# Performance work log

Hardware: AMD Instinct MI355X
Metric: run time of the kernel (lower is better)

## Reference

```python
import jax, jax.numpy as jnp
import numpy as np

EMBED_DIM = 256
NUM_HEADS = 4
HEAD_DIM = EMBED_DIM // NUM_HEADS
SCALE = HEAD_DIM ** (-0.5)


def setup_inputs() -> dict:
    key = jax.random.key(0)
    kx, kq, kp, kb = jax.random.split(key, 4)
    B, N, C = 4, 4096, EMBED_DIM
    x = jax.random.normal(kx, (B, N, C), dtype=jnp.float32)
    # qkv: Linear(C, 3C, bias=False); torch stores weight as [out, in]
    w_qkv = jax.random.normal(kq, (3 * C, C), dtype=jnp.float32) * (C ** -0.5)
    w_proj = jax.random.normal(kp, (C, C), dtype=jnp.float32) * (C ** -0.5)
    b_proj = jax.random.normal(kb, (C,), dtype=jnp.float32) * 0.01
    return {"x": x, "w_qkv": w_qkv, "w_proj": w_proj, "b_proj": b_proj}


def reference(x, w_qkv, w_proj, b_proj):
    B, N, C = x.shape
    H, D = NUM_HEADS, HEAD_DIM
    # qkv projection: [B,N,3C] -> [3,B,H,N,D]
    qkv = (x @ w_qkv.T).reshape(B, N, 3, H, D).transpose(2, 0, 3, 1, 4)
    q, k, v = qkv[0], qkv[1], qkv[2]
    # materialized [B,H,N,N] scores (faithful to the original)
    attn = jnp.einsum("bhnd,bhmd->bhnm", q, k) * SCALE
    attn_probs = jax.nn.softmax(attn, axis=-1)
    out = jnp.einsum("bhnm,bhmd->bhnd", attn_probs, v)
    out = out.transpose(0, 2, 1, 3).reshape(B, N, C)
    return out @ w_proj.T + b_proj
```

## Files before the change

kernel.cpp:

```cpp
#include <hip/hip_runtime.h>
#include <hip/hip_bf16.h>

typedef __hip_bfloat16 bf16;
typedef _Float16 f16;
typedef __attribute__((ext_vector_type(8))) short bf16x8;
typedef __attribute__((ext_vector_type(8))) _Float16 f16x8;
typedef __attribute__((ext_vector_type(2))) _Float16 f16x2;
typedef __attribute__((ext_vector_type(4))) float f32x4;
typedef __attribute__((ext_vector_type(4))) unsigned int u32x4;
typedef __attribute__((ext_vector_type(2))) unsigned int u32x2;

#define B_ 4
#define N_ 4096
#define C_ 256
#define H_ 4
#define D_ 64
#define KLN 0.18033688011112042f

#if __has_builtin(__builtin_amdgcn_exp2f)
#define EXP2(x) __builtin_amdgcn_exp2f(x)
#else
#define EXP2(x) exp2f(x)
#endif
#if __has_builtin(__builtin_amdgcn_rcpf)
#define RCP(x) __builtin_amdgcn_rcpf(x)
#else
#define RCP(x) (1.0f / (x))
#endif

__device__ inline void load_lds16(const void* g, void* l) {
#if __has_builtin(__builtin_amdgcn_global_load_lds)
    __builtin_amdgcn_global_load_lds(
        (const __attribute__((address_space(1))) unsigned int*)g,
        (__attribute__((address_space(3))) unsigned int*)l, 16, 0, 0);
#else
    int ln = __lane_id();
    ((u32x4*)l)[ln] = *((const u32x4*)g);
#endif
}

__device__ inline unsigned int pk2(float a, float b) {
    unsigned int ua = __builtin_bit_cast(unsigned int, a) + 0x8000u;
    unsigned int ub = __builtin_bit_cast(unsigned int, b) + 0x8000u;
    return (ua >> 16) | (ub & 0xffff0000u);
}
__device__ inline unsigned int pkh2(float a, float b) {
#if __has_builtin(__builtin_amdgcn_cvt_pkrtz)
    return __builtin_bit_cast(unsigned int, __builtin_amdgcn_cvt_pkrtz(a, b));
#else
    f16x2 h = { (f16)a, (f16)b };
    return __builtin_bit_cast(unsigned int, h);
#endif
}
__device__ inline short f2s(float x) {
    return (short)__builtin_bit_cast(unsigned short, __float2bfloat16(x));
}
__device__ inline bf16x8 cvt8(const float* __restrict__ p) {
    f32x4 a = *reinterpret_cast<const f32x4*>(p);
    f32x4 b = *reinterpret_cast<const f32x4*>(p + 4);
    bf16x8 r = { f2s(a[0]), f2s(a[1]), f2s(a[2]), f2s(a[3]),
                 f2s(b[0]), f2s(b[1]), f2s(b[2]), f2s(b[3]) };
    return r;
}

__global__ __launch_bounds__(256) void cast_bf16(const float* __restrict__ x,
                                                 const float* __restrict__ wq,
                                                 const float* __restrict__ wp,
                                                 bf16* __restrict__ xb,
                                                 bf16* __restrict__ wqb,
                                                 bf16* __restrict__ wpb)
{
    int bid = blockIdx.x;
    const float* s; bf16* d; int base;
    if (bid < 2048)      { s = x;  d = xb;  base = bid * 2048; }
    else if (bid < 2144) { s = wq; d = wqb; base = (bid - 2048) * 2048; }
    else                 { s = wp; d = wpb; base = (bid - 2144) * 2048; }
    int i = base + threadIdx.x * 8;
    f32x4 a = *reinterpret_cast<const f32x4*>(s + i);
    f32x4 b = *reinterpret_cast<const f32x4*>(s + i + 4);
    u32x4 o;
    o.x = pk2(a[0], a[1]); o.y = pk2(a[2], a[3]);
    o.z = pk2(b[0], b[1]); o.w = pk2(b[2], b[3]);
    *reinterpret_cast<u32x4*>(d + i) = o;
}

__global__ __launch_bounds__(256, 2) void qkv_fast(const bf16* __restrict__ x,
                                                   const bf16* __restrict__ w,
                                                   bf16* __restrict__ qw,
                                                   bf16* __restrict__ kw,
                                                   f16* __restrict__ vtw)
{
    __shared__ short w_s[64][264];
    const int tid  = threadIdx.x;
    const int lane = tid & 63;
    const int wav  = tid >> 6;
    const int quad = lane >> 4;
    const int l16  = lane & 15;
    const int bid = (blockIdx.x & 7) * 192 + (blockIdx.x >> 3);
    const int mt = bid / 12, nb = bid % 12;
    const int m0 = mt * 128, n0 = nb * 64;

    {
        const int row = tid >> 2, cb = (tid & 3) * 64;
        const bf16* src = w + (size_t)(n0 + row) * C_ + cb;
#pragma unroll
        for (int i = 0; i < 8; ++i)
            *reinterpret_cast<bf16x8*>(&w_s[row][cb + i * 8]) =
                *reinterpret_cast<const bf16x8*>(src + i * 8);
    }
    __syncthreads();

#pragma unroll
    for (int half = 0; half < 2; ++half) {
        const int mh = m0 + half * 64;
        f32x4 acc[4] = {{0,0,0,0},{0,0,0,0},{0,0,0,0},{0,0,0,0}};
        const bf16* xrow = x + (size_t)(mh + wav * 16 + l16) * C_ + quad * 8;
        if (nb < 8) {
#pragma unroll
            for (int k0 = 0; k0 < C_; k0 += 32) {
                bf16x8 a = *reinterpret_cast<const bf16x8*>(xrow + k0);
#pragma unroll
                for (int nt = 0; nt < 4; ++nt) {
                    bf16x8 b = *reinterpret_cast<const bf16x8*>(&w_s[nt * 16 + l16][k0 + quad * 8]);
                    acc[nt] = __builtin_amdgcn_mfma_f32_16x16x32_bf16(b, a, acc[nt], 0, 0, 0);
                }
            }
        } else {
#pragma unroll
            for (int k0 = 0; k0 < C_; k0 += 32) {
                bf16x8 a = *reinterpret_cast<const bf16x8*>(xrow + k0);
#pragma unroll
                for (int nt = 0; nt < 4; ++nt) {
                    bf16x8 b = *reinterpret_cast<const bf16x8*>(&w_s[nt * 16 + l16][k0 + quad * 8]);
                    acc[nt] = __builtin_amdgcn_mfma_f32_16x16x32_bf16(a, b, acc[nt], 0, 0, 0);
                }
            }
        }

        const int bb = mh >> 12;
        const int nbase = (mh + wav * 16) & (N_ - 1);
        if (nb < 4) {
            bf16* dst = qw + (((size_t)bb * H_ + nb) * N_ + nbase + l16) * D_;
#pragma unroll
            for (int nt = 0; nt < 4; ++nt) {
                u32x2 wv = { pk2(acc[nt][0] * KLN, acc[nt][1] * KLN),
                             pk2(acc[nt][2] * KLN, acc[nt][3] * KLN) };
                *reinterpret_cast<u32x2*>(dst + nt * 16 + quad * 4) = wv;
            }
        } else if (nb < 8) {
            bf16* dst = kw + (((size_t)bb * H_ + (nb - 4)) * N_ + nbase + l16) * D_;
#pragma unroll
            for (int nt = 0; nt < 4; ++nt) {
                u32x2 wv = { pk2(acc[nt][0], acc[nt][1]),
                             pk2(acc[nt][2], acc[nt][3]) };
                *reinterpret_cast<u32x2*>(dst + nt * 16 + quad * 4) = wv;
            }
        } else {
            const int h = nb - 8;
#pragma unroll
            for (int nt = 0; nt < 4; ++nt) {
                int d = nt * 16 + l16;
                u32x2 wv;
                wv.x = pkh2(acc[nt][0], acc[nt][1]);
                wv.y = pkh2(acc[nt][2], acc[nt][3]);
                *reinterpret_cast<u32x2*>(
                    vtw + (((size_t)bb * H_ + h) * D_ + d) * N_ + nbase + quad * 4) = wv;
            }
        }
    }
}

__global__ __launch_bounds__(256) void qkv_cvt(const float* __restrict__ x,
                                               const float* __restrict__ w,
                                               bf16* __restrict__ qw,
                                               bf16* __restrict__ kw,
                                               f16* __restrict__ vtw)
{
    const int lane = threadIdx.x & 63;
    const int wav  = threadIdx.x >> 6;
    const int quad = lane >> 4;
    const int l16  = lane & 15;
    const int gw   = blockIdx.x * 4 + wav;
    const int m0   = (gw / 12) * 16;
    const int n0   = (gw % 12) * 64;

    f32x4 acc[4] = {{0,0,0,0},{0,0,0,0},{0,0,0,0},{0,0,0,0}};
    const float* xrow = x + (size_t)(m0 + l16) * C_ + quad * 8;
#pragma unroll
    for (int k0 = 0; k0 < C_; k0 += 32) {
        bf16x8 a = cvt8(xrow + k0);
#pragma unroll
        for (int nt = 0; nt < 4; ++nt) {
            bf16x8 b = cvt8(w + (size_t)(n0 + nt * 16 + l16) * C_ + k0 + quad * 8);
            acc[nt] = __builtin_amdgcn_mfma_f32_16x16x32_bf16(a, b, acc[nt], 0, 0, 0);
        }
    }
#pragma unroll
    for (int nt = 0; nt < 4; ++nt)
#pragma unroll
        for (int r = 0; r < 4; ++r) {
            int m  = m0 + quad * 4 + r;
            int o  = n0 + nt * 16 + l16;
            int bb = m >> 12;
            int n  = m & (N_ - 1);
            if (o < 256) {
                int h = o >> 6, d = o & 63;
                qw[(((size_t)bb * H_ + h) * N_ + n) * D_ + d] =
                    __float2bfloat16(acc[nt][r] * KLN);
            } else if (o < 512) {
                int oo = o - 256; int h = oo >> 6, d = oo & 63;
                kw[(((size_t)bb * H_ + h) * N_ + n) * D_ + d] =
                    __float2bfloat16(acc[nt][r]);
            } else {
                int oo = o - 512; int h = oo >> 6, d = oo & 63;
                vtw[(((size_t)bb * H_ + h) * D_ + d) * N_ + n] = (f16)acc[nt][r];
            }
        }
}

__global__ __launch_bounds__(512, 4) void attn(const bf16* __restrict__ q,
                                               const bf16* __restrict__ k,
                                               const f16* __restrict__ vt,
                                               bf16* __restrict__ o)
{
    __shared__ __align__(16) char smem[65536];
    short* k_s = reinterpret_cast<short*>(smem);
    f16*   v_s = reinterpret_cast<f16*>(smem + 32768);

    const int tid  = threadIdx.x;
    const int lane = tid & 63;
    const int wav  = tid >> 6;
    const int quad = lane >> 4;
    const int l16  = lane & 15;
    const int l8   = lane & 7;
    const int sub  = wav & 3;
    const int jh   = wav >> 2;

    const int wg = (blockIdx.x & 7) * 64 + (blockIdx.x >> 3);
    const int bh = wg >> 5;
    const int qt = wg & 31;
    const int bb = bh >> 2, h = bh & 3;

    const bf16* qp = q  + (size_t)bh * N_ * D_;
    const bf16* kp = k  + (size_t)bh * N_ * D_;
    const f16*  vp = vt + (size_t)bh * D_ * N_;

    const int qbase = qt * 128 + sub * 32;
    bf16x8 qb[2][2];
#pragma unroll
    for (int qg = 0; qg < 2; ++qg)
#pragma unroll
        for (int ks = 0; ks < 2; ++ks)
            qb[qg][ks] = *reinterpret_cast<const bf16x8*>(
                qp + (size_t)(qbase + qg * 16 + l16) * D_ + ks * 32 + quad * 8);

    const int ri = lane >> 3;
    const int ci = lane & 7;
    const int gc = ci ^ ri;
    int koff[2], voff[2], lds_r[2];
#pragma unroll
    for (int g = 0; g < 2; ++g) {
        const int rb  = sub * 16 + g * 8;
        const int rho = rb + ri;
        const int pr  = (rho & 32) | ((rho & 12) << 1) | ((rho & 16) >> 2) | (rho & 3);
        koff[g]  = pr * D_ + gc * 8;
        voff[g]  = rho * N_ + gc * 8;
        lds_r[g] = rb * 64;
    }

    f32x4 oacc[2][4];
    f32x4 lv[2];
#pragma unroll
    for (int qg = 0; qg < 2; ++qg) {
        lv[qg] = (f32x4){0, 0, 0, 0};
#pragma unroll
        for (int dt = 0; dt < 4; ++dt) oacc[qg][dt] = (f32x4){0, 0, 0, 0};
    }

    auto stage = [&](int buf, int t) {
        const int j0 = jh * 2048 + t * 64;
        short* kd = k_s + (size_t)(buf * 2 + jh) * 4096;
        f16*   vd = v_s + (size_t)(buf * 2 + jh) * 4096;
#pragma unroll
        for (int g = 0; g < 2; ++g) {
            load_lds16(kp + (size_t)j0 * D_ + koff[g], kd + lds_r[g]);
            load_lds16(vp + j0 + voff[g],              vd + lds_r[g]);
        }
    };

    stage(0, 0);
    __syncthreads();

    for (int t = 0; t < 32; ++t) {
        const int cur = t & 1;
        if (t < 31) stage(cur ^ 1, t + 1);

        const short* kt  = k_s + (size_t)(cur * 2 + jh) * 4096;
        const f16*   vtl = v_s + (size_t)(cur * 2 + jh) * 4096;

        f32x4 s[2][4];
        __builtin_amdgcn_s_setprio(1);
#pragma unroll
        for (int nt = 0; nt < 4; ++nt) {
            const int rb = (nt * 16 + l16) * 64;
            bf16x8 k0 = *reinterpret_cast<const bf16x8*>(kt + rb + ((quad    ) ^ l8) * 8);
            bf16x8 k1 = *reinterpret_cast<const bf16x8*>(kt + rb + ((4 + quad) ^ l8) * 8);
#pragma unroll
            for (int qg = 0; qg < 2; ++qg) {
                s[qg][nt] = __builtin_amdgcn_mfma_f32_16x16x32_bf16(
                    k0, qb[qg][0], (f32x4){0.f, 0.f, 0.f, 0.f}, 0, 0, 0);
                s[qg][nt] = __builtin_amdgcn_mfma_f32_16x16x32_bf16(
                    k1, qb[qg][1], s[qg][nt], 0, 0, 0);
            }
        }
        __builtin_amdgcn_s_setprio(0);

        f16x8 pb[2][2];
#pragma unroll
        for (int qg = 0; qg < 2; ++qg)
#pragma unroll
            for (int ks = 0; ks < 2; ++ks) {
                const f32x4 sa = s[qg][2 * ks], sb = s[qg][2 * ks + 1];
                f32x4 pa = { EXP2(sa[0]), EXP2(sa[1]), EXP2(sa[2]), EXP2(sa[3]) };
                f32x4 pc = { EXP2(sb[0]), EXP2(sb[1]), EXP2(sb[2]), EXP2(sb[3]) };
                u32x4 pw;
                pw.x = pkh2(pa[0], pa[1]);
                pw.y = pkh2(pa[2], pa[3]);
                pw.z = pkh2(pc[0], pc[1]);
                pw.w = pkh2(pc[2], pc[3]);
                pb[qg][ks] = __builtin_bit_cast(f16x8, pw);
                lv[qg] += pa;
                lv[qg] += pc;
            }

        __builtin_amdgcn_s_setprio(1);
#pragma unroll
        for (int ks = 0; ks < 2; ++ks)
#pragma unroll
            for (int dt = 0; dt < 4; ++dt) {
                f16x8 va = *reinterpret_cast<const f16x8*>(
                    vtl + (dt * 16 + l16) * 64 + (((ks << 2) + quad) ^ l8) * 8);
#pragma unroll
                for (int qg = 0; qg < 2; ++qg)
                    oacc[qg][dt] = __builtin_amdgcn_mfma_f32_16x16x32_f16(va, pb[qg][ks], oacc[qg][dt], 0, 0, 0);
            }
        __builtin_amdgcn_s_setprio(0);

        __syncthreads();
    }

    float lr[2];
#pragma unroll
    for (int qg = 0; qg < 2; ++qg) {
        float l = (lv[qg][0] + lv[qg][1]) + (lv[qg][2] + lv[qg][3]);
        l += __shfl_xor(l, 16);
        l += __shfl_xor(l, 32);
        lr[qg] = l;
    }

    float* mrg = reinterpret_cast<float*>(smem);
    const int slot = (sub * 64 + lane) * 35;
    if (jh == 1) {
#pragma unroll
        for (int qg = 0; qg < 2; ++qg) {
#pragma unroll
            for (int dt = 0; dt < 4; ++dt)
#pragma unroll
                for (int e = 0; e < 4; ++e)
                    mrg[slot + qg * 17 + dt * 4 + e] = oacc[qg][dt][e];
            mrg[slot + qg * 17 + 16] = lr[qg];
        }
    }
    __syncthreads();
    if (jh == 0) {
#pragma unroll
        for (int qg = 0; qg < 2; ++qg) {
            const float rl = RCP(lr[qg] + mrg[slot + qg * 17 + 16]);
            const size_t obase = ((size_t)bb * N_ + qbase + qg * 16 + l16) * C_ + h * D_;
#pragma unroll
            for (int dt = 0; dt < 4; ++dt) {
                float v0 = (oacc[qg][dt][0] + mrg[slot + qg * 17 + dt * 4 + 0]) * rl;
                float v1 = (oacc[qg][dt][1] + mrg[slot + qg * 17 + dt * 4 + 1]) * rl;
                float v2 = (oacc[qg][dt][2] + mrg[slot + qg * 17 + dt * 4 + 2]) * rl;
                float v3 = (oacc[qg][dt][3] + mrg[slot + qg * 17 + dt * 4 + 3]) * rl;
                u32x2 wv = { pk2(v0, v1), pk2(v2, v3) };
                *reinterpret_cast<u32x2*>(o + obase + dt * 16 + quad * 4) = wv;
            }
        }
    }
}

__global__ __launch_bounds__(256, 2) void out_proj_fast(const bf16* __restrict__ ov,
                                                        const bf16* __restrict__ w,
                                                        const float* __restrict__ bias,
                                                        float* __restrict__ out)
{
    __shared__ short w_s[64][264];
    const int tid  = threadIdx.x;
    const int lane = tid & 63;
    const int wav  = tid >> 6;
    const int quad = lane >> 4;
    const int l16  = lane & 15;
    const int bid = (blockIdx.x & 7) * 64 + (blockIdx.x >> 3);
    const int m0 = (bid >> 2) * 128;
    const int n0 = (bid & 3) * 64;

    {
        const int row = tid >> 2, cb = (tid & 3) * 64;
        const bf16* src = w + (size_t)(n0 + row) * C_ + cb;
#pragma unroll
        for (int i = 0; i < 8; ++i)
            *reinterpret_cast<bf16x8*>(&w_s[row][cb + i * 8]) =
                *reinterpret_cast<const bf16x8*>(src + i * 8);
    }
    __syncthreads();

#pragma unroll
    for (int half = 0; half < 2; ++half) {
        const int mh = m0 + half * 64;
        f32x4 acc[4] = {{0,0,0,0},{0,0,0,0},{0,0,0,0},{0,0,0,0}};
        const bf16* orow = ov + (size_t)(mh + wav * 16 + l16) * C_ + quad * 8;
#pragma unroll
        for (int k0 = 0; k0 < C_; k0 += 32) {
            bf16x8 a = *reinterpret_cast<const bf16x8*>(orow + k0);
#pragma unroll
            for (int nt = 0; nt < 4; ++nt) {
                bf16x8 b = *reinterpret_cast<const bf16x8*>(&w_s[nt * 16 + l16][k0 + quad * 8]);
                acc[nt] = __builtin_amdgcn_mfma_f32_16x16x32_bf16(b, a, acc[nt], 0, 0, 0);
            }
        }
        const int m = mh + wav * 16 + l16;
#pragma unroll
        for (int nt = 0; nt < 4; ++nt) {
            const int oc0 = n0 + nt * 16 + quad * 4;
            f32x4 bv = *reinterpret_cast<const f32x4*>(bias + oc0);
            f32x4 ovv = acc[nt] + bv;
            *reinterpret_cast<f32x4*>(out + (size_t)m * C_ + oc0) = ovv;
        }
    }
}

__global__ __launch_bounds__(256) void out_proj_cvt(const bf16* __restrict__ ov,
                                                    const float* __restrict__ w,
                                                    const float* __restrict__ bias,
                                                    float* __restrict__ out)
{
    const int lane = threadIdx.x & 63;
    const int wav  = threadIdx.x >> 6;
    const int quad = lane >> 4;
    const int l16  = lane & 15;
    const int gw   = blockIdx.x * 4 + wav;
    const int m0   = (gw >> 2) * 16;
    const int n0   = (gw & 3) * 64;

    f32x4 acc[4] = {{0,0,0,0},{0,0,0,0},{0,0,0,0},{0,0,0,0}};
    const bf16* orow = ov + (size_t)(m0 + l16) * C_ + quad * 8;
#pragma unroll
    for (int k0 = 0; k0 < C_; k0 += 32) {
        bf16x8 a = *reinterpret_cast<const bf16x8*>(orow + k0);
#pragma unroll
        for (int nt = 0; nt < 4; ++nt) {
            bf16x8 b = cvt8(w + (size_t)(n0 + nt * 16 + l16) * C_ + k0 + quad * 8);
            acc[nt] = __builtin_amdgcn_mfma_f32_16x16x32_bf16(a, b, acc[nt], 0, 0, 0);
        }
    }
#pragma unroll
    for (int nt = 0; nt < 4; ++nt)
#pragma unroll
        for (int r = 0; r < 4; ++r) {
            int m  = m0 + quad * 4 + r;
            int oc = n0 + nt * 16 + l16;
            out[(size_t)m * C_ + oc] = acc[nt][r] + bias[oc];
        }
}

extern "C" void kernel_launch(void* const* d_in, const int* in_sizes, int n_in,
                              void* d_out, int out_size, void* d_ws, size_t ws_size,
                              hipStream_t stream) {
    const float* x      = (const float*)d_in[0];
    const float* w_qkv  = (const float*)d_in[1];
    const float* w_proj = (const float*)d_in[2];
    const float* b_proj = (const float*)d_in[3];
    float* out = (float*)d_out;

    const size_t qkv_elems = (size_t)B_ * H_ * N_ * D_;
    bf16* q_ws  = (bf16*)d_ws;
    bf16* k_ws  = q_ws  + qkv_elems;
    f16*  vt_ws = (f16*)(k_ws + qkv_elems);
    bf16* o_ws  = (bf16*)(vt_ws + qkv_elems);
    bf16* x_bf  = o_ws  + qkv_elems;
    bf16* wq_bf = x_bf  + (size_t)B_ * N_ * C_;
    bf16* wp_bf = wq_bf + (size_t)3 * C_ * C_;

    const size_t need = ((size_t)4 * qkv_elems + (size_t)B_ * N_ * C_
                         + (size_t)3 * C_ * C_ + (size_t)C_ * C_) * 2;

    if (ws_size >= need) {
        cast_bf16    <<<2176, 256, 0, stream>>>(x, w_qkv, w_proj, x_bf, wq_bf, wp_bf);
        qkv_fast     <<<1536, 256, 0, stream>>>(x_bf, wq_bf, q_ws, k_ws, vt_ws);
        attn         <<< 512, 512, 0, stream>>>(q_ws, k_ws, vt_ws, o_ws);
        out_proj_fast<<< 512, 256, 0, stream>>>(o_ws, wp_bf, b_proj, out);
    } else {
        qkv_cvt      <<<3072, 256, 0, stream>>>(x, w_qkv, q_ws, k_ws, vt_ws);
        attn         <<< 512, 512, 0, stream>>>(q_ws, k_ws, vt_ws, o_ws);
        out_proj_cvt <<<1024, 256, 0, stream>>>(o_ws, w_proj, b_proj, out);
    }
}
```

Measured before the change: 174.9 us.

## Halve attention waves per block and give each wave 64 query rows

The attention block now runs 4 waves instead of 8, so each wave owns 64 query rows (four 16-row groups) rather than 32. Every K and V fragment read from LDS then feeds twice as many MFMAs, which cuts LDS traffic per unit of work. The exp2 and pack step is now interleaved directly after each QK MFMA pair instead of running as a separate pass, and the s_setprio hints are removed. In exchange, each wave holds more accumulator registers and each CU has fewer waves in flight to hide latency.

```diff
diff --git a/kernel.cpp b/kernel.cpp
--- a/kernel.cpp
+++ b/kernel.cpp
@@ -218,7 +218,7 @@
         }
 }
 
-__global__ __launch_bounds__(512, 4) void attn(const bf16* __restrict__ q,
+__global__ __launch_bounds__(256, 2) void attn(const bf16* __restrict__ q,
                                                const bf16* __restrict__ k,
                                                const f16* __restrict__ vt,
                                                bf16* __restrict__ o)
@@ -233,8 +233,8 @@
     const int quad = lane >> 4;
     const int l16  = lane & 15;
     const int l8   = lane & 7;
-    const int sub  = wav & 3;
-    const int jh   = wav >> 2;
+    const int sub  = wav & 1;
+    const int jh   = wav >> 1;
 
     const int wg = (blockIdx.x & 7) * 64 + (blockIdx.x >> 3);
     const int bh = wg >> 5;
@@ -245,10 +245,10 @@
     const bf16* kp = k  + (size_t)bh * N_ * D_;
     const f16*  vp = vt + (size_t)bh * D_ * N_;
 
-    const int qbase = qt * 128 + sub * 32;
-    bf16x8 qb[2][2];
-#pragma unroll
-    for (int qg = 0; qg < 2; ++qg)
+    const int qbase = qt * 128 + sub * 64;
+    bf16x8 qb[4][2];
+#pragma unroll
+    for (int qg = 0; qg < 4; ++qg)
 #pragma unroll
         for (int ks = 0; ks < 2; ++ks)
             qb[qg][ks] = *reinterpret_cast<const bf16x8*>(
@@ -257,10 +257,10 @@
     const int ri = lane >> 3;
     const int ci = lane & 7;
     const int gc = ci ^ ri;
-    int koff[2], voff[2], lds_r[2];
-#pragma unroll
-    for (int g = 0; g < 2; ++g) {
-        const int rb  = sub * 16 + g * 8;
+    int koff[4], voff[4], lds_r[4];
+#pragma unroll
+    for (int g = 0; g < 4; ++g) {
+        const int rb  = sub * 32 + g * 8;
         const int rho = rb + ri;
         const int pr  = (rho & 32) | ((rho & 12) << 1) | ((rho & 16) >> 2) | (rho & 3);
         koff[g]  = pr * D_ + gc * 8;
@@ -268,10 +268,10 @@
         lds_r[g] = rb * 64;
     }
 
-    f32x4 oacc[2][4];
-    f32x4 lv[2];
-#pragma unroll
-    for (int qg = 0; qg < 2; ++qg) {
+    f32x4 oacc[4][4];
+    f32x4 lv[4];
+#pragma unroll
+    for (int qg = 0; qg < 4; ++qg) {
         lv[qg] = (f32x4){0, 0, 0, 0};
 #pragma unroll
         for (int dt = 0; dt < 4; ++dt) oacc[qg][dt] = (f32x4){0, 0, 0, 0};
@@ -282,7 +282,7 @@
         short* kd = k_s + (size_t)(buf * 2 + jh) * 4096;
         f16*   vd = v_s + (size_t)(buf * 2 + jh) * 4096;
 #pragma unroll
-        for (int g = 0; g < 2; ++g) {
+        for (int g = 0; g < 4; ++g) {
             load_lds16(kp + (size_t)j0 * D_ + koff[g], kd + lds_r[g]);
             load_lds16(vp + j0 + voff[g],              vd + lds_r[g]);
         }
@@ -298,42 +298,28 @@
         const short* kt  = k_s + (size_t)(cur * 2 + jh) * 4096;
         const f16*   vtl = v_s + (size_t)(cur * 2 + jh) * 4096;
 
-        f32x4 s[2][4];
-        __builtin_amdgcn_s_setprio(1);
+        f16x8 pb[4][2];
 #pragma unroll
         for (int nt = 0; nt < 4; ++nt) {
             const int rb = (nt * 16 + l16) * 64;
             bf16x8 k0 = *reinterpret_cast<const bf16x8*>(kt + rb + ((quad    ) ^ l8) * 8);
             bf16x8 k1 = *reinterpret_cast<const bf16x8*>(kt + rb + ((4 + quad) ^ l8) * 8);
 #pragma unroll
-            for (int qg = 0; qg < 2; ++qg) {
-                s[qg][nt] = __builtin_amdgcn_mfma_f32_16x16x32_bf16(
+            for (int qg = 0; qg < 4; ++qg) {
+                f32x4 sv = __builtin_amdgcn_mfma_f32_16x16x32_bf16(
                     k0, qb[qg][0], (f32x4){0.f, 0.f, 0.f, 0.f}, 0, 0, 0);
-                s[qg][nt] = __builtin_amdgcn_mfma_f32_16x16x32_bf16(
-                    k1, qb[qg][1], s[qg][nt], 0, 0, 0);
-            }
-        }
-        __builtin_amdgcn_s_setprio(0);
-
-        f16x8 pb[2][2];
-#pragma unroll
-        for (int qg = 0; qg < 2; ++qg)
-#pragma unroll
-            for (int ks = 0; ks < 2; ++ks) {
-                const f32x4 sa = s[qg][2 * ks], sb = s[qg][2 * ks + 1];
-                f32x4 pa = { EXP2(sa[0]), EXP2(sa[1]), EXP2(sa[2]), EXP2(sa[3]) };
-                f32x4 pc = { EXP2(sb[0]), EXP2(sb[1]), EXP2(sb[2]), EXP2(sb[3]) };
-                u32x4 pw;
-                pw.x = pkh2(pa[0], pa[1]);
-                pw.y = pkh2(pa[2], pa[3]);
-                pw.z = pkh2(pc[0], pc[1]);
-                pw.w = pkh2(pc[2], pc[3]);
-                pb[qg][ks] = __builtin_bit_cast(f16x8, pw);
+                sv = __builtin_amdgcn_mfma_f32_16x16x32_bf16(
+                    k1, qb[qg][1], sv, 0, 0, 0);
+                f32x4 pa = { EXP2(sv[0]), EXP2(sv[1]), EXP2(sv[2]), EXP2(sv[3]) };
+                u32x2 pw = { pkh2(pa[0], pa[1]), pkh2(pa[2], pa[3]) };
+                if (nt & 1)
+                    *(reinterpret_cast<u32x2*>(&pb[qg][nt >> 1]) + 1) = pw;
+                else
+                    *(reinterpret_cast<u32x2*>(&pb[qg][nt >> 1]) + 0) = pw;
                 lv[qg] += pa;
-                lv[qg] += pc;
-            }
-
-        __builtin_amdgcn_s_setprio(1);
+            }
+        }
+
 #pragma unroll
         for (int ks = 0; ks < 2; ++ks)
 #pragma unroll
@@ -341,17 +327,16 @@
                 f16x8 va = *reinterpret_cast<const f16x8*>(
                     vtl + (dt * 16 + l16) * 64 + (((ks << 2) + quad) ^ l8) * 8);
 #pragma unroll
-                for (int qg = 0; qg < 2; ++qg)
+                for (int qg = 0; qg < 4; ++qg)
                     oacc[qg][dt] = __builtin_amdgcn_mfma_f32_16x16x32_f16(va, pb[qg][ks], oacc[qg][dt], 0, 0, 0);
             }
-        __builtin_amdgcn_s_setprio(0);
 
         __syncthreads();
     }
 
-    float lr[2];
-#pragma unroll
-    for (int qg = 0; qg < 2; ++qg) {
+    float lr[4];
+#pragma unroll
+    for (int qg = 0; qg < 4; ++qg) {
         float l = (lv[qg][0] + lv[qg][1]) + (lv[qg][2] + lv[qg][3]);
         l += __shfl_xor(l, 16);
         l += __shfl_xor(l, 32);
@@ -359,10 +344,10 @@
     }
 
     float* mrg = reinterpret_cast<float*>(smem);
-    const int slot = (sub * 64 + lane) * 35;
+    const int slot = (sub * 64 + lane) * 69;
     if (jh == 1) {
 #pragma unroll
-        for (int qg = 0; qg < 2; ++qg) {
+        for (int qg = 0; qg < 4; ++qg) {
 #pragma unroll
             for (int dt = 0; dt < 4; ++dt)
 #pragma unroll
@@ -374,7 +359,7 @@
     __syncthreads();
     if (jh == 0) {
 #pragma unroll
-        for (int qg = 0; qg < 2; ++qg) {
+        for (int qg = 0; qg < 4; ++qg) {
             const float rl = RCP(lr[qg] + mrg[slot + qg * 17 + 16]);
             const size_t obase = ((size_t)bb * N_ + qbase + qg * 16 + l16) * C_ + h * D_;
 #pragma unroll
@@ -498,11 +483,11 @@
     if (ws_size >= need) {
         cast_bf16    <<<2176, 256, 0, stream>>>(x, w_qkv, w_proj, x_bf, wq_bf, wp_bf);
         qkv_fast     <<<1536, 256, 0, stream>>>(x_bf, wq_bf, q_ws, k_ws, vt_ws);
-        attn         <<< 512, 512, 0, stream>>>(q_ws, k_ws, vt_ws, o_ws);
+        attn         <<< 512, 256, 0, stream>>>(q_ws, k_ws, vt_ws, o_ws);
         out_proj_fast<<< 512, 256, 0, stream>>>(o_ws, wp_bf, b_proj, out);
     } else {
         qkv_cvt      <<<3072, 256, 0, stream>>>(x, w_qkv, q_ws, k_ws, vt_ws);
-        attn         <<< 512, 512, 0, stream>>>(q_ws, k_ws, vt_ws, o_ws);
+        attn         <<< 512, 256, 0, stream>>>(q_ws, k_ws, vt_ws, o_ws);
         out_proj_cvt <<<1024, 256, 0, stream>>>(o_ws, w_proj, b_proj, out);
     }
 }
```

Result: no change. 174.8 us (-0.1%).
